# Kernel tuning notes

Measured on AMD Instinct MI355X. Metric: run time of the kernel, lower is better.

## Reference

```python
import jax, jax.numpy as jnp
import numpy as np
from jax import lax

# Rotation permutations for a flattened 3x3 kernel (row-major, new_flat[t] = orig_flat[perm[t]]),
# transcribed literally from _rotate_kernel for n = angle//45 in {0,1,2,3}.
PERMS = np.array([
    [0, 1, 2, 3, 4, 5, 6, 7, 8],  # 0 deg (identity)
    [3, 0, 1, 6, 4, 2, 7, 8, 5],  # 45 deg: outer ring shifted one step
    [6, 3, 0, 7, 4, 1, 8, 5, 2],  # 90 deg clockwise
    [7, 6, 3, 8, 4, 0, 5, 2, 1],  # 135 deg
], dtype=np.int32)


def setup_inputs() -> dict:
    key = jax.random.key(0)
    k1, k2, k3 = jax.random.split(key, 3)
    B, Cin, Cout, H, W = 16, 64, 64, 128, 128
    x = jax.random.normal(k1, (B, Cin, H, W), dtype=jnp.float32)
    weight = jax.random.normal(k2, (Cout, Cin, 3, 3), dtype=jnp.float32)
    bias = jax.random.normal(k3, (Cout, 1, 1), dtype=jnp.float32)
    return {"x": x, "weight": weight, "bias": bias}


def reference(x, weight, bias):
    # x: [B, Cin, H, W]; weight: [Cout, Cin, 3, 3]; bias: [Cout, 1, 1]
    B, Cin, H, W = x.shape
    Cout = weight.shape[0]
    n_ang = PERMS.shape[0]

    # Build the 4 rotated kernel variants in one gather.
    wflat = weight.reshape(Cout, Cin, 9)
    # [Cout, Cin, n_ang, 9] -> [n_ang, Cout, Cin, 3, 3] -> merge angle into output channels
    wrot = wflat[:, :, jnp.asarray(PERMS)].transpose(2, 0, 1, 3).reshape(n_ang * Cout, Cin, 3, 3)

    # ZeroPad2d(stride=1) then valid 3x3 conv -> same spatial size.
    xp = jnp.pad(x, ((0, 0), (0, 0), (1, 1), (1, 1)))
    y = lax.conv_general_dilated(
        xp, wrot, window_strides=(1, 1), padding="VALID",
        dimension_numbers=("NCHW", "OIHW", "NCHW"))  # [B, n_ang*Cout, H, W]

    y = y.reshape(B, n_ang, Cout, H, W).transpose(1, 0, 2, 3, 4)  # [n_ang, B, Cout, H, W]
    return y + bias  # bias (Cout,1,1) broadcasts over trailing dims
```

## Files before the change

### kernel.cpp

```cpp
#include <hip/hip_runtime.h>


#define CIN 64
#define COUT 64
#define HH 128
#define WW 128
#define NB 16
#define HW (HH*WW)

typedef short bf16x8 __attribute__((ext_vector_type(8)));
typedef float f32x16 __attribute__((ext_vector_type(16)));
#define AS1 __attribute__((address_space(1)))
#define AS3 __attribute__((address_space(3)))

__device__ __constant__ unsigned char DHI_d[4][9] = {
  {0,0,0,1,1,1,2,2,2},
  {0,0,1,0,1,2,1,2,2},
  {0,1,2,0,1,2,0,1,2},
  {1,2,2,0,1,2,0,0,1},
};
__device__ __constant__ unsigned short DWB_d[4][9] = {
  {0,16,32,0,16,32,0,16,32},
  {16,32,32,0,16,32,0,0,16},
  {32,32,32,16,16,16,0,0,0},
  {32,32,16,32,16,0,16,0,0},
};

static __device__ __forceinline__ unsigned short f2bf(float f) {
  unsigned u = __builtin_bit_cast(unsigned, f);
  return (unsigned short)((u + 0x7FFFu + ((u >> 16) & 1u)) >> 16);
}
static __device__ __forceinline__ unsigned pk2(float lo, float hi) {
  return (unsigned)f2bf(lo) | ((unsigned)f2bf(hi) << 16);
}

__global__ __launch_bounds__(256) void xt_build_kernel(const float* __restrict__ x,
                                                       unsigned short* __restrict__ xt) {
  const int gid = blockIdx.x * 256 + threadIdx.x;
  const int w = gid & 127;
  const int h = (gid >> 7) & 127;
  const int slot = (gid >> 14) & 7;
  const int b = gid >> 17;
  const float* xp = x + ((size_t)(b * CIN + slot * 8) * HH + h) * WW + w;
  uint4 u;
  u.x = pk2(xp[0], xp[HW]);
  u.y = pk2(xp[2 * HW], xp[3 * HW]);
  u.z = pk2(xp[4 * HW], xp[5 * HW]);
  u.w = pk2(xp[6 * HW], xp[7 * HW]);
  const size_t idx = ((size_t)(b * HH + h) * 8 + slot) * 128 + w;
  *(uint4*)((unsigned char*)xt + idx * 16) = u;
}

__global__ void build_A_kernel(const float* __restrict__ wgt,
                               const float* __restrict__ bias,
                               unsigned short* __restrict__ A) {
  const int e = blockIdx.x * 256 + threadIdx.x;
  const int j = e & 7;
  const int cm = (e >> 3) & 63;
  const int half = (e >> 9) & 1;
  const int kc = e >> 10;
  if (kc < 36) {
    const int s = kc >> 2, q = kc & 3;
    const int ci = q * 16 + half * 8 + j;
    A[e] = f2bf(wgt[(cm * CIN + ci) * 9 + s]);
  } else if (kc == 36) {
    A[e] = (half == 0 && j == 0) ? f2bf(bias[cm]) : (unsigned short)0;
  }
}

#define V9_SLOT 2080
#define V9_ROW  16640
#define V9_XOFF 75776
#define V9_LDS  (V9_XOFF + 4 * V9_ROW)

__global__ __launch_bounds__(1024, 4) void aconv_v9_kernel(
    const unsigned short* __restrict__ xt,
    const unsigned short* __restrict__ Ag,
    float* __restrict__ out)
{
  __shared__ __align__(16) unsigned char lds[V9_LDS];

  const int tid = threadIdx.x;
  const int lane = tid & 63;
  const int wid = tid >> 6;
  const int a   = wid >> 2;
  const int row = (wid >> 1) & 1;
  const int wh  = wid & 1;
  const int half = lane >> 5;
  const int ln = lane & 31;

  const int b   = blockIdx.x >> 4;
  const int rem = blockIdx.x & 15;
  const int hbase = rem * 8;

  const unsigned char* Agb = (const unsigned char*)Ag;
  const unsigned char* xtb = (const unsigned char*)xt;
  AS3 unsigned char* ldsa = (AS3 unsigned char*)lds;
  const uint4 z4 = {0u, 0u, 0u, 0u};

  #pragma unroll
  for (int j = 0; j < 5; ++j) {
    const int i = wid + j * 16;
    if (i < 74)
      __builtin_amdgcn_global_load_lds(
          (const AS1 unsigned*)(Agb + i * 1024 + lane * 16),
          (AS3 unsigned*)(ldsa + i * 1024), 16, 0, 0);
  }
  if (tid < 64) {
    const int rs = tid >> 4, cs = (tid >> 1) & 7, side = tid & 1;
    *(uint4*)(lds + V9_XOFF + rs * V9_ROW + cs * V9_SLOT + side * 129 * 16) = z4;
  }
  #pragma unroll
  for (int j = 0; j < 4; ++j) {
    const int c = wid + j * 16;
    const int rr = c >> 4;
    const int s  = (c >> 1) & 7;
    const int k  = c & 1;
    const int gh = hbase - 1 + rr;
    const unsigned dst = (unsigned)(V9_XOFF + rr * V9_ROW + s * V9_SLOT + 16 + k * 1024);
    if (gh >= 0) {
      __builtin_amdgcn_global_load_lds(
          (const AS1 unsigned*)(xtb + ((size_t)((b * HH + gh) * 8 + s) * 128 + k * 64) * 16 + lane * 16),
          (AS3 unsigned*)(ldsa + dst), 16, 0, 0);
    } else {
      *(uint4*)(lds + dst + lane * 16) = z4;
    }
  }
  __syncthreads();

  const unsigned char* Asb = lds + (unsigned)(half * 1024 + ln * 16);
  const unsigned char* Bsb = lds + V9_XOFF + (unsigned)(half * V9_SLOT + (wh * 64 + ln) * 16);

  bf16x8 ob = (bf16x8)(short)0;
  if (half == 0) ob[0] = (short)0x3F80;

  #pragma unroll 1
  for (int it = 0; it < 4; ++it) {
    unsigned boff_t[9];
    #pragma unroll
    for (int s = 0; s < 9; ++s)
      boff_t[s] = (unsigned)DWB_d[a][s]
                + (unsigned)(((it * 2 + row + (int)DHI_d[a][s]) & 3) * V9_ROW);

    f32x16 acc[2][2];
    #pragma unroll
    for (int mf = 0; mf < 2; ++mf)
      #pragma unroll
      for (int nf = 0; nf < 2; ++nf) acc[mf][nf] = (f32x16)(0.f);

    #pragma unroll
    for (int kc = 0; kc < 36; ++kc) {
      const bf16x8 af0 = *(const bf16x8*)(Asb + kc * 2048);
      const bf16x8 af1 = *(const bf16x8*)(Asb + kc * 2048 + 512);
      const unsigned bb = boff_t[kc >> 2] + (unsigned)((kc & 3) * 2 * V9_SLOT);
      const bf16x8 bf0 = *(const bf16x8*)(Bsb + bb);
      const bf16x8 bf1 = *(const bf16x8*)(Bsb + bb + 512);
      acc[0][0] = __builtin_amdgcn_mfma_f32_32x32x16_bf16(af0, bf0, acc[0][0], 0, 0, 0);
      acc[0][1] = __builtin_amdgcn_mfma_f32_32x32x16_bf16(af0, bf1, acc[0][1], 0, 0, 0);
      acc[1][0] = __builtin_amdgcn_mfma_f32_32x32x16_bf16(af1, bf0, acc[1][0], 0, 0, 0);
      acc[1][1] = __builtin_amdgcn_mfma_f32_32x32x16_bf16(af1, bf1, acc[1][1], 0, 0, 0);
    }
    {
      const bf16x8 af0 = *(const bf16x8*)(Asb + 36 * 2048);
      const bf16x8 af1 = *(const bf16x8*)(Asb + 36 * 2048 + 512);
      acc[0][0] = __builtin_amdgcn_mfma_f32_32x32x16_bf16(af0, ob, acc[0][0], 0, 0, 0);
      acc[0][1] = __builtin_amdgcn_mfma_f32_32x32x16_bf16(af0, ob, acc[0][1], 0, 0, 0);
      acc[1][0] = __builtin_amdgcn_mfma_f32_32x32x16_bf16(af1, ob, acc[1][0], 0, 0, 0);
      acc[1][1] = __builtin_amdgcn_mfma_f32_32x32x16_bf16(af1, ob, acc[1][1], 0, 0, 0);
    }

    const int hout = hbase + it * 2 + row;
    #pragma unroll
    for (int mf = 0; mf < 2; ++mf)
      #pragma unroll
      for (int nf = 0; nf < 2; ++nf) {
        const f32x16 v = acc[mf][nf];
        float* op = out + (((size_t)(a * NB + b) * COUT + mf * 32 + 4 * half) * HH
                           + hout) * WW + wh * 64 + nf * 32 + ln;
        #pragma unroll
        for (int g = 0; g < 16; ++g)
          __builtin_nontemporal_store(v[g], op + (size_t)((g & 3) + 8 * (g >> 2)) * HW);
      }

    asm volatile("s_waitcnt lgkmcnt(0)" ::: "memory");
    __builtin_amdgcn_s_barrier();

    if (it < 3) {
      #pragma unroll
      for (int j = 0; j < 2; ++j) {
        const int c = wid + j * 16;
        const int rr = c >> 4;
        const int s  = (c >> 1) & 7;
        const int k  = c & 1;
        const int gh = hbase + it * 2 + 3 + rr;
        const unsigned dst = (unsigned)(V9_XOFF + ((it * 2 + rr) & 3) * V9_ROW
                                        + s * V9_SLOT + 16 + k * 1024);
        if (gh < HH) {
          __builtin_amdgcn_global_load_lds(
              (const AS1 unsigned*)(xtb + ((size_t)((b * HH + gh) * 8 + s) * 128 + k * 64) * 16 + lane * 16),
              (AS3 unsigned*)(ldsa + dst), 16, 0, 0);
        } else {
          *(uint4*)(lds + dst + lane * 16) = z4;
        }
      }
      asm volatile("s_waitcnt vmcnt(0) lgkmcnt(0)" ::: "memory");
      __builtin_amdgcn_s_barrier();
    }
  }
}

#define R7_SLOT 1072
#define R7_ROW  8576
#define R7_XOFF 73728
#define R7_LDS  (R7_XOFF + 4 * R7_ROW)

static __device__ __forceinline__ void lgkm_barrier() {
  asm volatile("s_waitcnt lgkmcnt(0)" ::: "memory");
  __builtin_amdgcn_s_barrier();
}

__global__ __launch_bounds__(512) void aconv_v7_kernel(
    const float* __restrict__ x,
    const unsigned short* __restrict__ Ag,
    const float* __restrict__ bias,
    float* __restrict__ out)
{
  __shared__ __align__(16) unsigned char lds[R7_LDS];

  const int tid = threadIdx.x;
  const int lane = tid & 63;
  const int wid = tid >> 6;
  const int a   = wid >> 1;
  const int row = wid & 1;
  const int half = lane >> 5;
  const int ln = lane & 31;

  const int blk = blockIdx.x;
  const int b   = blk >> 4;
  const int rem = blk & 15;
  const int hbase = rem * 8;

  float bv[2][16];
  #pragma unroll
  for (int mf = 0; mf < 2; ++mf)
    #pragma unroll
    for (int g = 0; g < 16; ++g)
      bv[mf][g] = bias[mf * 32 + (g & 3) + 8 * (g >> 2) + 4 * half];

  int dhi[9]; unsigned dwb[9];
  #pragma unroll
  for (int s = 0; s < 9; ++s) { dhi[s] = DHI_d[a][s]; dwb[s] = DWB_d[a][s]; }

  {
    const uint4* Ag4 = (const uint4*)Ag;
    uint4* As4 = (uint4*)lds;
    #pragma unroll
    for (int i = 0; i < 9; ++i) As4[tid + i * 512] = Ag4[tid + i * 512];
  }

  float gv[5][8];
  unsigned gdst[5];
  bool gval[5];

  #pragma unroll
  for (int i = 0; i < 5; ++i) {
    const int g = tid + i * 512;
    const bool v = g < 2112;
    const int rg = g / 528;
    const int rest = g - rg * 528;
    const int slot = rest / 66;
    const int wI = rest - slot * 66;
    const int hx = hbase - 1 + rg;
    const int gw = -1 + wI;
    const bool inb = v && ((unsigned)hx < HH) && ((unsigned)gw < WW);
    const float* xp = x + (size_t)(b * CIN + slot * 8) * HW + (size_t)hx * WW + gw;
    gval[i] = v;
    gdst[i] = (unsigned)(R7_XOFF + rg * R7_ROW + slot * R7_SLOT + wI * 16);
    #pragma unroll
    for (int q = 0; q < 8; ++q) gv[i][q] = inb ? xp[(size_t)q * HW] : 0.f;
  }
  #pragma unroll
  for (int i = 0; i < 5; ++i)
    if (gval[i]) {
      uint4 u;
      u.x = pk2(gv[i][0], gv[i][1]); u.y = pk2(gv[i][2], gv[i][3]);
      u.z = pk2(gv[i][4], gv[i][5]); u.w = pk2(gv[i][6], gv[i][7]);
      *(uint4*)(lds + gdst[i]) = u;
    }
  __syncthreads();

  const unsigned char* Asb = lds + (unsigned)(half * 1024 + ln * 16);
  const unsigned char* Bsb = lds + R7_XOFF + (unsigned)(half * R7_SLOT + ln * 16);

  #pragma unroll 1
  for (int ti = 0; ti < 8; ++ti) {
    const int wh = ti >> 2, it = ti & 3;
    const int w0 = wh * 64;

    unsigned boff_t[9];
    {
      unsigned rowoff[3];
      #pragma unroll
      for (int dh = 0; dh < 3; ++dh)
        rowoff[dh] = (unsigned)(((2 * it + row + dh) & 3) * R7_ROW);
      #pragma unroll
      for (int s = 0; s < 9; ++s) boff_t[s] = dwb[s] + rowoff[dhi[s]];
    }

    const bool pf2 = (it < 3);
    const bool pf4 = (it == 3) && (wh == 0);
    const int ngran = pf2 ? 1056 : (pf4 ? 2112 : 0);
    if (ngran) {
      const int itv = pf4 ? -2 : it;
      const int w0n = pf4 ? 64 : w0;
      #pragma unroll
      for (int i = 0; i < 5; ++i) {
        const int g = tid + i * 512;
        const bool v = g < ngran;
        const int rg = g / 528;
        const int rest = g - rg * 528;
        const int slot = rest / 66;
        const int wI = rest - slot * 66;
        const int hx = hbase + 2 * itv + 3 + rg;
        const int ps = (2 * itv + 4 + rg) & 3;
        const int gw = w0n - 1 + wI;
        const bool inb = v && ((unsigned)hx < HH) && ((unsigned)gw < WW);
        const float* xp = x + (size_t)(b * CIN + slot * 8) * HW + (size_t)hx * WW + gw;
        gval[i] = v;
        gdst[i] = (unsigned)(R7_XOFF + ps * R7_ROW + slot * R7_SLOT + wI * 16);
        #pragma unroll
        for (int q = 0; q < 8; ++q) gv[i][q] = inb ? xp[(size_t)q * HW] : 0.f;
      }
    }

    f32x16 acc[2][2];
    #pragma unroll
    for (int mf = 0; mf < 2; ++mf)
      #pragma unroll
      for (int nf = 0; nf < 2; ++nf)
        #pragma unroll
        for (int g = 0; g < 16; ++g)
          acc[mf][nf][g] = bv[mf][g];

    #pragma unroll
    for (int kc = 0; kc < 36; ++kc) {
      const bf16x8 af0 = *(const bf16x8*)(Asb + kc * 2048);
      const bf16x8 af1 = *(const bf16x8*)(Asb + kc * 2048 + 512);
      const unsigned bb = boff_t[kc >> 2] + (unsigned)((kc & 3) * 2 * R7_SLOT);
      const bf16x8 bf0 = *(const bf16x8*)(Bsb + bb);
      const bf16x8 bf1 = *(const bf16x8*)(Bsb + bb + 512);
      acc[0][0] = __builtin_amdgcn_mfma_f32_32x32x16_bf16(af0, bf0, acc[0][0], 0, 0, 0);
      acc[0][1] = __builtin_amdgcn_mfma_f32_32x32x16_bf16(af0, bf1, acc[0][1], 0, 0, 0);
      acc[1][0] = __builtin_amdgcn_mfma_f32_32x32x16_bf16(af1, bf0, acc[1][0], 0, 0, 0);
      acc[1][1] = __builtin_amdgcn_mfma_f32_32x32x16_bf16(af1, bf1, acc[1][1], 0, 0, 0);
    }

    const int hout = hbase + it * 2 + row;
    #pragma unroll
    for (int mf = 0; mf < 2; ++mf)
      #pragma unroll
      for (int nf = 0; nf < 2; ++nf) {
        const f32x16 v = acc[mf][nf];
        float* op = out + (((size_t)(a * NB + b) * COUT + mf * 32 + 4 * half) * HH
                           + hout) * WW + w0 + nf * 32 + ln;
        #pragma unroll
        for (int g = 0; g < 16; ++g)
          __builtin_nontemporal_store(v[g], op + (size_t)((g & 3) + 8 * (g >> 2)) * HW);
      }

    lgkm_barrier();
    if (ngran) {
      #pragma unroll
      for (int i = 0; i < 5; ++i)
        if (gval[i]) {
          uint4 u;
          u.x = pk2(gv[i][0], gv[i][1]); u.y = pk2(gv[i][2], gv[i][3]);
          u.z = pk2(gv[i][4], gv[i][5]); u.w = pk2(gv[i][6], gv[i][7]);
          *(uint4*)(lds + gdst[i]) = u;
        }
    }
    lgkm_barrier();
  }
}

extern "C" void kernel_launch(void* const* d_in, const int* in_sizes, int n_in,
                              void* d_out, int out_size, void* d_ws, size_t ws_size,
                              hipStream_t stream) {
  const float* x    = (const float*)d_in[0];
  const float* wgt  = (const float*)d_in[1];
  const float* bias = (const float*)d_in[2];
  float* out = (float*)d_out;

  const size_t XT_BYTES = (size_t)NB * HH * 8 * 128 * 16;
  const size_t A_BYTES  = 75776;

  if (ws_size >= XT_BYTES + A_BYTES) {
    unsigned short* xt = (unsigned short*)d_ws;
    unsigned short* A  = (unsigned short*)((char*)d_ws + XT_BYTES);
    build_A_kernel<<<148, 256, 0, stream>>>(wgt, bias, A);
    xt_build_kernel<<<8192, 256, 0, stream>>>(x, xt);
    aconv_v9_kernel<<<256, 1024, 0, stream>>>(xt, A, out);
  } else {
    unsigned short* A = (unsigned short*)d_ws;
    build_A_kernel<<<148, 256, 0, stream>>>(wgt, bias, A);
    aconv_v7_kernel<<<256, 512, 0, stream>>>(x, A, bias, out);
  }
}
```

Before: 119.4 us.

## Halve block to 8 waves with 2x4 MFMA tiles and prefetch fragments

Switches the conv kernel from 16 waves per block to 8, so each wave now covers a full 128-wide output row with a 2x4 grid of 32x32 MFMA accumulators instead of 2x2. Each A fragment is reused across twice as many B fragments, which cuts LDS reads per MFMA. The inner loop also software-pipelines the LDS fragment loads one K-step ahead so they overlap with the MFMAs. The cost is doubled accumulator registers (128 floats per lane) plus the prefetch buffers, and half as many waves per block to hide latency.

```diff
diff --git a/kernel.cpp b/kernel.cpp
--- a/kernel.cpp
+++ b/kernel.cpp
@@ -73,7 +73,7 @@
 #define V9_XOFF 75776
 #define V9_LDS  (V9_XOFF + 4 * V9_ROW)
 
-__global__ __launch_bounds__(1024, 4) void aconv_v9_kernel(
+__global__ __launch_bounds__(512, 2) void aconv_v10_kernel(
     const unsigned short* __restrict__ xt,
     const unsigned short* __restrict__ Ag,
     float* __restrict__ out)
@@ -83,9 +83,8 @@
   const int tid = threadIdx.x;
   const int lane = tid & 63;
   const int wid = tid >> 6;
-  const int a   = wid >> 2;
-  const int row = (wid >> 1) & 1;
-  const int wh  = wid & 1;
+  const int a   = wid >> 1;
+  const int row = wid & 1;
   const int half = lane >> 5;
   const int ln = lane & 31;
 
@@ -99,8 +98,8 @@
   const uint4 z4 = {0u, 0u, 0u, 0u};
 
   #pragma unroll
-  for (int j = 0; j < 5; ++j) {
-    const int i = wid + j * 16;
+  for (int j = 0; j < 10; ++j) {
+    const int i = wid + j * 8;
     if (i < 74)
       __builtin_amdgcn_global_load_lds(
           (const AS1 unsigned*)(Agb + i * 1024 + lane * 16),
@@ -111,8 +110,8 @@
     *(uint4*)(lds + V9_XOFF + rs * V9_ROW + cs * V9_SLOT + side * 129 * 16) = z4;
   }
   #pragma unroll
-  for (int j = 0; j < 4; ++j) {
-    const int c = wid + j * 16;
+  for (int j = 0; j < 8; ++j) {
+    const int c = wid + j * 8;
     const int rr = c >> 4;
     const int s  = (c >> 1) & 7;
     const int k  = c & 1;
@@ -129,7 +128,7 @@
   __syncthreads();
 
   const unsigned char* Asb = lds + (unsigned)(half * 1024 + ln * 16);
-  const unsigned char* Bsb = lds + V9_XOFF + (unsigned)(half * V9_SLOT + (wh * 64 + ln) * 16);
+  const unsigned char* Bsb = lds + V9_XOFF + (unsigned)(half * V9_SLOT + ln * 16);
 
   bf16x8 ob = (bf16x8)(short)0;
   if (half == 0) ob[0] = (short)0x3F80;
@@ -142,41 +141,62 @@
       boff_t[s] = (unsigned)DWB_d[a][s]
                 + (unsigned)(((it * 2 + row + (int)DHI_d[a][s]) & 3) * V9_ROW);
 
-    f32x16 acc[2][2];
+    f32x16 acc[2][4];
     #pragma unroll
     for (int mf = 0; mf < 2; ++mf)
       #pragma unroll
-      for (int nf = 0; nf < 2; ++nf) acc[mf][nf] = (f32x16)(0.f);
+      for (int nf = 0; nf < 4; ++nf) acc[mf][nf] = (f32x16)(0.f);
+
+    bf16x8 ca0 = *(const bf16x8*)(Asb);
+    bf16x8 ca1 = *(const bf16x8*)(Asb + 512);
+    unsigned bb0 = boff_t[0];
+    bf16x8 cb0 = *(const bf16x8*)(Bsb + bb0);
+    bf16x8 cb1 = *(const bf16x8*)(Bsb + bb0 + 512);
+    bf16x8 cb2 = *(const bf16x8*)(Bsb + bb0 + 1024);
+    bf16x8 cb3 = *(const bf16x8*)(Bsb + bb0 + 1536);
 
     #pragma unroll
     for (int kc = 0; kc < 36; ++kc) {
-      const bf16x8 af0 = *(const bf16x8*)(Asb + kc * 2048);
-      const bf16x8 af1 = *(const bf16x8*)(Asb + kc * 2048 + 512);
-      const unsigned bb = boff_t[kc >> 2] + (unsigned)((kc & 3) * 2 * V9_SLOT);
-      const bf16x8 bf0 = *(const bf16x8*)(Bsb + bb);
-      const bf16x8 bf1 = *(const bf16x8*)(Bsb + bb + 512);
-      acc[0][0] = __builtin_amdgcn_mfma_f32_32x32x16_bf16(af0, bf0, acc[0][0], 0, 0, 0);
-      acc[0][1] = __builtin_amdgcn_mfma_f32_32x32x16_bf16(af0, bf1, acc[0][1], 0, 0, 0);
-      acc[1][0] = __builtin_amdgcn_mfma_f32_32x32x16_bf16(af1, bf0, acc[1][0], 0, 0, 0);
-      acc[1][1] = __builtin_amdgcn_mfma_f32_32x32x16_bf16(af1, bf1, acc[1][1], 0, 0, 0);
+      bf16x8 na0, na1, nb0, nb1, nb2, nb3;
+      if (kc < 35) {
+        const int kn = kc + 1;
+        na0 = *(const bf16x8*)(Asb + kn * 2048);
+        na1 = *(const bf16x8*)(Asb + kn * 2048 + 512);
+        const unsigned bb = boff_t[kn >> 2] + (unsigned)((kn & 3) * 2 * V9_SLOT);
+        nb0 = *(const bf16x8*)(Bsb + bb);
+        nb1 = *(const bf16x8*)(Bsb + bb + 512);
+        nb2 = *(const bf16x8*)(Bsb + bb + 1024);
+        nb3 = *(const bf16x8*)(Bsb + bb + 1536);
+      } else {
+        na0 = *(const bf16x8*)(Asb + 36 * 2048);
+        na1 = *(const bf16x8*)(Asb + 36 * 2048 + 512);
+      }
+      acc[0][0] = __builtin_amdgcn_mfma_f32_32x32x16_bf16(ca0, cb0, acc[0][0], 0, 0, 0);
+      acc[1][0] = __builtin_amdgcn_mfma_f32_32x32x16_bf16(ca1, cb0, acc[1][0], 0, 0, 0);
+      acc[0][1] = __builtin_amdgcn_mfma_f32_32x32x16_bf16(ca0, cb1, acc[0][1], 0, 0, 0);
+      acc[1][1] = __builtin_amdgcn_mfma_f32_32x32x16_bf16(ca1, cb1, acc[1][1], 0, 0, 0);
+      acc[0][2] = __builtin_amdgcn_mfma_f32_32x32x16_bf16(ca0, cb2, acc[0][2], 0, 0, 0);
+      acc[1][2] = __builtin_amdgcn_mfma_f32_32x32x16_bf16(ca1, cb2, acc[1][2], 0, 0, 0);
+      acc[0][3] = __builtin_amdgcn_mfma_f32_32x32x16_bf16(ca0, cb3, acc[0][3], 0, 0, 0);
+      acc[1][3] = __builtin_amdgcn_mfma_f32_32x32x16_bf16(ca1, cb3, acc[1][3], 0, 0, 0);
+      ca0 = na0; ca1 = na1; cb0 = nb0; cb1 = nb1; cb2 = nb2; cb3 = nb3;
     }
     {
-      const bf16x8 af0 = *(const bf16x8*)(Asb + 36 * 2048);
-      const bf16x8 af1 = *(const bf16x8*)(Asb + 36 * 2048 + 512);
-      acc[0][0] = __builtin_amdgcn_mfma_f32_32x32x16_bf16(af0, ob, acc[0][0], 0, 0, 0);
-      acc[0][1] = __builtin_amdgcn_mfma_f32_32x32x16_bf16(af0, ob, acc[0][1], 0, 0, 0);
-      acc[1][0] = __builtin_amdgcn_mfma_f32_32x32x16_bf16(af1, ob, acc[1][0], 0, 0, 0);
-      acc[1][1] = __builtin_amdgcn_mfma_f32_32x32x16_bf16(af1, ob, acc[1][1], 0, 0, 0);
+      #pragma unroll
+      for (int nf = 0; nf < 4; ++nf) {
+        acc[0][nf] = __builtin_amdgcn_mfma_f32_32x32x16_bf16(ca0, ob, acc[0][nf], 0, 0, 0);
+        acc[1][nf] = __builtin_amdgcn_mfma_f32_32x32x16_bf16(ca1, ob, acc[1][nf], 0, 0, 0);
+      }
     }
 
     const int hout = hbase + it * 2 + row;
     #pragma unroll
     for (int mf = 0; mf < 2; ++mf)
       #pragma unroll
-      for (int nf = 0; nf < 2; ++nf) {
+      for (int nf = 0; nf < 4; ++nf) {
         const f32x16 v = acc[mf][nf];
         float* op = out + (((size_t)(a * NB + b) * COUT + mf * 32 + 4 * half) * HH
-                           + hout) * WW + wh * 64 + nf * 32 + ln;
+                           + hout) * WW + nf * 32 + ln;
         #pragma unroll
         for (int g = 0; g < 16; ++g)
           __builtin_nontemporal_store(v[g], op + (size_t)((g & 3) + 8 * (g >> 2)) * HW);
@@ -187,8 +207,8 @@
 
     if (it < 3) {
       #pragma unroll
-      for (int j = 0; j < 2; ++j) {
-        const int c = wid + j * 16;
+      for (int j = 0; j < 4; ++j) {
+        const int c = wid + j * 8;
         const int rr = c >> 4;
         const int s  = (c >> 1) & 7;
         const int k  = c & 1;
@@ -399,7 +419,7 @@
     unsigned short* A  = (unsigned short*)((char*)d_ws + XT_BYTES);
     build_A_kernel<<<148, 256, 0, stream>>>(wgt, bias, A);
     xt_build_kernel<<<8192, 256, 0, stream>>>(x, xt);
-    aconv_v9_kernel<<<256, 1024, 0, stream>>>(xt, A, out);
+    aconv_v10_kernel<<<256, 512, 0, stream>>>(xt, A, out);
   } else {
     unsigned short* A = (unsigned short*)d_ws;
     build_A_kernel<<<148, 256, 0, stream>>>(wgt, bias, A);
```

After: 124.0 us. +3.8%, slower.

## Reorder tap loop by input row and overlap row prefetch with MFMA

Applied to the files above, without the earlier changes.

The 3x3 taps are now visited in input-row order, with a per-angle table giving the permuted weight-slab offsets, so the first three taps touch only rows already resident. The next-row global-to-LDS prefetch is issued before the output stores, and the wait for it is moved to a barrier after the third tap of the following iteration rather than a full vmcnt(0) wait. This lets the row loads overlap the stores and the first compute phase. It depends on the 'vmcnt(63)' wait and the ring-buffer row indexing being correct; any mistake there means reading stale LDS rows.

```diff
diff --git a/kernel.cpp b/kernel.cpp
--- a/kernel.cpp
+++ b/kernel.cpp
@@ -13,6 +13,18 @@
 #define AS1 __attribute__((address_space(1)))
 #define AS3 __attribute__((address_space(3)))
 
+__device__ __constant__ unsigned AOFF_d[4][9] = {
+  {0, 8192, 16384, 24576, 32768, 40960, 49152, 57344, 65536},
+  {0, 8192, 24576, 16384, 32768, 49152, 40960, 57344, 65536},
+  {0, 24576, 49152, 8192, 32768, 57344, 16384, 40960, 65536},
+  {24576, 49152, 57344, 0, 32768, 65536, 8192, 16384, 40960},
+};
+__device__ __constant__ unsigned short DWBS_d[4][9] = {
+  {0,16,32, 0,16,32, 0,16,32},
+  {16,32,0, 32,16,0, 32,0,16},
+  {32,16,0, 32,16,0, 32,16,0},
+  {32,16,0, 32,16,0, 32,16,0},
+};
 __device__ __constant__ unsigned char DHI_d[4][9] = {
   {0,0,0,1,1,1,2,2,2},
   {0,0,1,0,1,2,1,2,2},
@@ -73,7 +85,7 @@
 #define V9_XOFF 75776
 #define V9_LDS  (V9_XOFF + 4 * V9_ROW)
 
-__global__ __launch_bounds__(1024, 4) void aconv_v9_kernel(
+__global__ __launch_bounds__(1024, 4) void aconv_v11_kernel(
     const unsigned short* __restrict__ xt,
     const unsigned short* __restrict__ Ag,
     float* __restrict__ out)
@@ -97,6 +109,10 @@
   const unsigned char* xtb = (const unsigned char*)xt;
   AS3 unsigned char* ldsa = (AS3 unsigned char*)lds;
   const uint4 z4 = {0u, 0u, 0u, 0u};
+
+  unsigned aoff[9]; unsigned short dwbs[9];
+  #pragma unroll
+  for (int j = 0; j < 9; ++j) { aoff[j] = AOFF_d[a][j]; dwbs[j] = DWBS_d[a][j]; }
 
   #pragma unroll
   for (int j = 0; j < 5; ++j) {
@@ -138,9 +154,9 @@
   for (int it = 0; it < 4; ++it) {
     unsigned boff_t[9];
     #pragma unroll
-    for (int s = 0; s < 9; ++s)
-      boff_t[s] = (unsigned)DWB_d[a][s]
-                + (unsigned)(((it * 2 + row + (int)DHI_d[a][s]) & 3) * V9_ROW);
+    for (int j = 0; j < 9; ++j)
+      boff_t[j] = (unsigned)dwbs[j]
+                + (unsigned)(((it * 2 + row + (j / 3)) & 3) * V9_ROW);
 
     f32x16 acc[2][2];
     #pragma unroll
@@ -149,16 +165,23 @@
       for (int nf = 0; nf < 2; ++nf) acc[mf][nf] = (f32x16)(0.f);
 
     #pragma unroll
-    for (int kc = 0; kc < 36; ++kc) {
-      const bf16x8 af0 = *(const bf16x8*)(Asb + kc * 2048);
-      const bf16x8 af1 = *(const bf16x8*)(Asb + kc * 2048 + 512);
-      const unsigned bb = boff_t[kc >> 2] + (unsigned)((kc & 3) * 2 * V9_SLOT);
-      const bf16x8 bf0 = *(const bf16x8*)(Bsb + bb);
-      const bf16x8 bf1 = *(const bf16x8*)(Bsb + bb + 512);
-      acc[0][0] = __builtin_amdgcn_mfma_f32_32x32x16_bf16(af0, bf0, acc[0][0], 0, 0, 0);
-      acc[0][1] = __builtin_amdgcn_mfma_f32_32x32x16_bf16(af0, bf1, acc[0][1], 0, 0, 0);
-      acc[1][0] = __builtin_amdgcn_mfma_f32_32x32x16_bf16(af1, bf0, acc[1][0], 0, 0, 0);
-      acc[1][1] = __builtin_amdgcn_mfma_f32_32x32x16_bf16(af1, bf1, acc[1][1], 0, 0, 0);
+    for (int j = 0; j < 9; ++j) {
+      if (j == 3) {
+        asm volatile("s_waitcnt vmcnt(63)" ::: "memory");
+        __builtin_amdgcn_s_barrier();
+      }
+      #pragma unroll
+      for (int q = 0; q < 4; ++q) {
+        const bf16x8 af0 = *(const bf16x8*)(Asb + aoff[j] + q * 2048);
+        const bf16x8 af1 = *(const bf16x8*)(Asb + aoff[j] + q * 2048 + 512);
+        const unsigned bb = boff_t[j] + (unsigned)(q * 2 * V9_SLOT);
+        const bf16x8 bf0 = *(const bf16x8*)(Bsb + bb);
+        const bf16x8 bf1 = *(const bf16x8*)(Bsb + bb + 512);
+        acc[0][0] = __builtin_amdgcn_mfma_f32_32x32x16_bf16(af0, bf0, acc[0][0], 0, 0, 0);
+        acc[0][1] = __builtin_amdgcn_mfma_f32_32x32x16_bf16(af0, bf1, acc[0][1], 0, 0, 0);
+        acc[1][0] = __builtin_amdgcn_mfma_f32_32x32x16_bf16(af1, bf0, acc[1][0], 0, 0, 0);
+        acc[1][1] = __builtin_amdgcn_mfma_f32_32x32x16_bf16(af1, bf1, acc[1][1], 0, 0, 0);
+      }
     }
     {
       const bf16x8 af0 = *(const bf16x8*)(Asb + 36 * 2048);
@@ -168,19 +191,6 @@
       acc[1][0] = __builtin_amdgcn_mfma_f32_32x32x16_bf16(af1, ob, acc[1][0], 0, 0, 0);
       acc[1][1] = __builtin_amdgcn_mfma_f32_32x32x16_bf16(af1, ob, acc[1][1], 0, 0, 0);
     }
-
-    const int hout = hbase + it * 2 + row;
-    #pragma unroll
-    for (int mf = 0; mf < 2; ++mf)
-      #pragma unroll
-      for (int nf = 0; nf < 2; ++nf) {
-        const f32x16 v = acc[mf][nf];
-        float* op = out + (((size_t)(a * NB + b) * COUT + mf * 32 + 4 * half) * HH
-                           + hout) * WW + wh * 64 + nf * 32 + ln;
-        #pragma unroll
-        for (int g = 0; g < 16; ++g)
-          __builtin_nontemporal_store(v[g], op + (size_t)((g & 3) + 8 * (g >> 2)) * HW);
-      }
 
     asm volatile("s_waitcnt lgkmcnt(0)" ::: "memory");
     __builtin_amdgcn_s_barrier();
@@ -203,9 +213,20 @@
           *(uint4*)(lds + dst + lane * 16) = z4;
         }
       }
-      asm volatile("s_waitcnt vmcnt(0) lgkmcnt(0)" ::: "memory");
-      __builtin_amdgcn_s_barrier();
-    }
+    }
+
+    const int hout = hbase + it * 2 + row;
+    #pragma unroll
+    for (int mf = 0; mf < 2; ++mf)
+      #pragma unroll
+      for (int nf = 0; nf < 2; ++nf) {
+        const f32x16 v = acc[mf][nf];
+        float* op = out + (((size_t)(a * NB + b) * COUT + mf * 32 + 4 * half) * HH
+                           + hout) * WW + wh * 64 + nf * 32 + ln;
+        #pragma unroll
+        for (int g = 0; g < 16; ++g)
+          __builtin_nontemporal_store(v[g], op + (size_t)((g & 3) + 8 * (g >> 2)) * HW);
+      }
   }
 }
 
@@ -399,7 +420,7 @@
     unsigned short* A  = (unsigned short*)((char*)d_ws + XT_BYTES);
     build_A_kernel<<<148, 256, 0, stream>>>(wgt, bias, A);
     xt_build_kernel<<<8192, 256, 0, stream>>>(x, xt);
-    aconv_v9_kernel<<<256, 1024, 0, stream>>>(xt, A, out);
+    aconv_v11_kernel<<<256, 1024, 0, stream>>>(xt, A, out);
   } else {
     unsigned short* A = (unsigned short*)d_ws;
     build_A_kernel<<<148, 256, 0, stream>>>(wgt, bias, A);
```

Measured after the change: 111.3 us. -6.8%, faster.
